# Performance work log

Hardware: AMD Instinct MI355X
Metric: run time of the kernel (lower is better)

The kernel has to match this reference:

```python
import jax, jax.numpy as jnp
import numpy as np

EPS = 1e-06
TOP_K = 2


def setup_inputs() -> dict:
    key = jax.random.key(0)
    k1, k2 = jax.random.split(key)
    B, S, H, E = 4, 4096, 2048, 64
    x = jax.random.normal(k1, (B, S, H), dtype=jnp.float32)
    per_dim_scale = jnp.ones((H,), dtype=jnp.float32)
    W = jax.random.normal(k2, (H, E), dtype=jnp.float32) * 0.02  # Dense kernel [H, E]
    return {"x": x, "per_dim_scale": per_dim_scale, "W": W}


def reference(x, per_dim_scale, W):
    H = x.shape[-1]
    x_flat = x.reshape(-1, H)  # [T, H]
    # Parameter-free RMSNorm (Gemma4VNorm)
    normed = x_flat * jax.lax.rsqrt(jnp.mean(jnp.square(x_flat), axis=-1, keepdims=True) + EPS)
    # scale by 1/sqrt(H), then learnable per-dim scale
    normed = normed * jnp.asarray(H, normed.dtype) ** -0.5
    normed = normed * per_dim_scale.astype(normed.dtype)
    router_logits = normed @ W  # [T, E]
    router_probs = jax.nn.softmax(router_logits.astype(jnp.float32), axis=-1).astype(x.dtype)
    top_k_probs, top_k_indices = jax.lax.top_k(router_probs, TOP_K)  # [T, k]
    denom = jnp.maximum(jnp.sum(top_k_probs, axis=-1, keepdims=True),
                        jnp.asarray(1e-09, top_k_probs.dtype))
    top_k_probs = top_k_probs / denom
    # Sparse dispatch weights [T, E] (sum of scaled one-hots == scatter-add)
    T = router_probs.shape[0]
    rows = jnp.arange(T)[:, None]  # [T, 1] broadcast against [T, k]
    dispatch_weights = jnp.zeros_like(router_probs).at[rows, top_k_indices].add(top_k_probs)
    return dispatch_weights
```

## Files before the change

kernel.cpp:

```cpp
#include <hip/hip_runtime.h>
#include <math.h>

#define H 2048
#define E 64
#define TAU 1e-6f

#define MT 16
#define KS 128
#define NSTEP (H / KS)
#define LPITCH 136

#define RB 16
#define CB 512
#define NCH (H / CB)
#define PITCH 516

#define WHI_OFF 65792u
#define WFRAG_BYTES 262144u
#define WLO_OFF (WHI_OFF + WFRAG_BYTES)
#define WS_NEEDED ((size_t)(WLO_OFF + WFRAG_BYTES))

typedef __attribute__((ext_vector_type(8))) short short8;
typedef __attribute__((ext_vector_type(4))) float f32x4;

__device__ __forceinline__ unsigned short bf16_rne(float f) {
    unsigned u = __float_as_uint(f);
    unsigned r = u + 0x7fffu + ((u >> 16) & 1u);
    return (unsigned short)(r >> 16);
}

__global__ __launch_bounds__(256)
void prep_w(const float* __restrict__ Wm, int* __restrict__ flags,
            unsigned short* __restrict__ whi, unsigned short* __restrict__ wlo)
{
    const int tid = blockIdx.x * 256 + threadIdx.x;
    if (tid == 0) flags[0] = 0;
    const int lane = tid & 63;
    const int fb   = tid >> 6;
    const int kc   = fb >> 2;
    const int n    = fb & 3;
    const int r0   = kc * 32 + (lane >> 4) * 8;
    const int col  = n * 16 + (lane & 15);

    short8 hv, lv;
#pragma unroll
    for (int j = 0; j < 8; ++j) {
        const float w = Wm[(r0 + j) * E + col];
        const unsigned short hb = bf16_rne(w);
        const float hf = __uint_as_float((unsigned)hb << 16);
        const unsigned short lb = bf16_rne(w - hf);
        hv[j] = (short)hb;
        lv[j] = (short)lb;
    }
    *(short8*)(whi + (size_t)tid * 8) = hv;
    *(short8*)(wlo + (size_t)tid * 8) = lv;
}

__global__ __launch_bounds__(256, 2)
void router_mfma16(const float* __restrict__ x,
                   const float* __restrict__ pds,
                   const unsigned short* __restrict__ whi,
                   const unsigned short* __restrict__ wlo,
                   float* __restrict__ out,
                   int* __restrict__ flags)
{
    __shared__ __align__(16) unsigned short yhi[MT * LPITCH];
    __shared__ __align__(16) unsigned short ylo[MT * LPITCH];
    __shared__ float lbuf[MT * E];
    __shared__ float ssbuf[256];
    __shared__ float sfac[MT];

    const int t    = threadIdx.x;
    const int wid  = t >> 6;
    const int lane = t & 63;
    const int row0 = blockIdx.x * MT;

    const int srow = t >> 4;
    const int scol = (t & 15) * 8;
    const float* xrow = x + (size_t)(row0 + srow) * H;

    f32x4 acc = {0.f, 0.f, 0.f, 0.f};
    float sumsq = 0.0f;

    float4 xv0 = *(const float4*)(xrow + scol);
    float4 xv1 = *(const float4*)(xrow + scol + 4);

    short8 whA[4], wlA[4], whB[4], wlB[4];
#pragma unroll
    for (int kk = 0; kk < 4; ++kk) {
        const size_t off = (((size_t)(kk * 4 + wid)) * 64 + lane) * 8;
        whA[kk] = *(const short8*)(whi + off);
        wlA[kk] = *(const short8*)(wlo + off);
    }

    auto body = [&](int c, short8 (&WH)[4], short8 (&WL)[4],
                           short8 (&NH)[4], short8 (&NL)[4]) {
        const int cn = (c + 1 < NSTEP) ? c + 1 : c;
#pragma unroll
        for (int kk = 0; kk < 4; ++kk) {
            const size_t off = (((size_t)((cn * 4 + kk) * 4 + wid)) * 64 + lane) * 8;
            NH[kk] = *(const short8*)(whi + off);
            NL[kk] = *(const short8*)(wlo + off);
        }

        const float* pb = pds + c * KS + scol;
        const float4 p0 = *(const float4*)(pb);
        const float4 p1 = *(const float4*)(pb + 4);
        sumsq += xv0.x * xv0.x + xv0.y * xv0.y + xv0.z * xv0.z + xv0.w * xv0.w
               + xv1.x * xv1.x + xv1.y * xv1.y + xv1.z * xv1.z + xv1.w * xv1.w;
        float y[8] = { xv0.x * p0.x, xv0.y * p0.y, xv0.z * p0.z, xv0.w * p0.w,
                       xv1.x * p1.x, xv1.y * p1.y, xv1.z * p1.z, xv1.w * p1.w };
        short8 hv, lv;
#pragma unroll
        for (int e = 0; e < 8; ++e) {
            const unsigned short hb = bf16_rne(y[e]);
            const unsigned short lb = bf16_rne(y[e] - __uint_as_float((unsigned)hb << 16));
            hv[e] = (short)hb;
            lv[e] = (short)lb;
        }
        *(short8*)(&yhi[srow * LPITCH + scol]) = hv;
        *(short8*)(&ylo[srow * LPITCH + scol]) = lv;
        __syncthreads();

        const int cx = (c + 1 < NSTEP) ? c + 1 : c;
        xv0 = *(const float4*)(xrow + cx * KS + scol);
        xv1 = *(const float4*)(xrow + cx * KS + scol + 4);

        const int abase = (lane & 15) * LPITCH + (lane >> 4) * 8;
#pragma unroll
        for (int kk = 0; kk < 4; ++kk) {
            const short8 ah = *(const short8*)(&yhi[abase + kk * 32]);
            const short8 al = *(const short8*)(&ylo[abase + kk * 32]);
            acc = __builtin_amdgcn_mfma_f32_16x16x32_bf16(ah, WH[kk], acc, 0, 0, 0);
            acc = __builtin_amdgcn_mfma_f32_16x16x32_bf16(ah, WL[kk], acc, 0, 0, 0);
            acc = __builtin_amdgcn_mfma_f32_16x16x32_bf16(al, WH[kk], acc, 0, 0, 0);
        }
        __syncthreads();
    };

    for (int c = 0; c < NSTEP; c += 2) {
        body(c,     whA, wlA, whB, wlB);
        body(c + 1, whB, wlB, whA, wlA);
    }

    ssbuf[t] = sumsq;
    __syncthreads();
    if (t < MT) {
        float tot = 0.0f;
#pragma unroll
        for (int i = 0; i < 16; ++i) tot += ssbuf[t * 16 + i];
        sfac[t] = rsqrtf(tot * (1.0f / (float)H) + 1e-6f) * 0.022097086912079608f;
    }

#pragma unroll
    for (int q = 0; q < 4; ++q)
        lbuf[(((lane >> 4) * 4) + q) * E + wid * 16 + (lane & 15)] = acc[q];
    __syncthreads();

#pragma unroll
    for (int rr = 0; rr < 4; ++rr) {
        const int r = wid * 4 + rr;
        const float L = lbuf[r * E + lane] * sfac[r];

        float m = L;
#pragma unroll
        for (int off = 32; off >= 1; off >>= 1)
            m = fmaxf(m, __shfl_xor(m, off));
        const float ev = expf(L - m);
        float S = ev;
#pragma unroll
        for (int off = 32; off >= 1; off >>= 1)
            S += __shfl_xor(S, off);
        const float p = ev / S;

        float v1 = p; int i1 = lane;
#pragma unroll
        for (int off = 32; off >= 1; off >>= 1) {
            const float ov = __shfl_xor(v1, off);
            const int   oi = __shfl_xor(i1, off);
            if (ov > v1 || (ov == v1 && oi < i1)) { v1 = ov; i1 = oi; }
        }
        float v2 = (lane == i1) ? -1.0f : p; int i2 = lane;
#pragma unroll
        for (int off = 32; off >= 1; off >>= 1) {
            const float ov = __shfl_xor(v2, off);
            const int   oi = __shfl_xor(i2, off);
            if (ov > v2 || (ov == v2 && oi < i2)) { v2 = ov; i2 = oi; }
        }
        float v3 = (lane == i1 || lane == i2) ? -1.0f : p;
#pragma unroll
        for (int off = 32; off >= 1; off >>= 1)
            v3 = fmaxf(v3, __shfl_xor(v3, off));

        if (lane == 0 && (v2 - v3) < TAU) {
            const int k = atomicAdd(flags, 1);
            flags[1 + k] = row0 + r;
        }

        const float denom = fmaxf(v1 + v2, 1e-9f);
        const float wA = v1 / denom;
        const float wB = v2 / denom;
        const float o  = (lane == i1) ? wA : ((lane == i2) ? wB : 0.0f);
        out[(size_t)(row0 + r) * E + lane] = o;
    }
}

__global__ __launch_bounds__(256)
void router_fix(const float* __restrict__ x,
                const float* __restrict__ pds,
                const float* __restrict__ Wm,
                float* __restrict__ out,
                const int* __restrict__ flags)
{
    __shared__ double yd[H];
    __shared__ double parts[4 * E];
    __shared__ double ss[256];

    const int t = threadIdx.x;
    const int count = flags[0];

    for (int j = blockIdx.x; j < count; j += gridDim.x) {
        const int r = flags[1 + j];
        const float* xr = x + (size_t)r * H;

        double s = 0.0;
#pragma unroll
        for (int i = 0; i < 8; ++i) {
            const int h = t * 8 + i;
            const double xv = (double)xr[h];
            s += xv * xv;
            yd[h] = xv * (double)pds[h];
        }
        ss[t] = s;
        __syncthreads();

        const int ex = t & 63;
        const int sl = t >> 6;
        const float* wp = Wm + (size_t)(sl * 512) * E + ex;
        double acc = 0.0;
#pragma unroll 8
        for (int h = 0; h < 512; ++h)
            acc = fma(yd[sl * 512 + h], (double)wp[(size_t)h * E], acc);
        parts[sl * E + ex] = acc;
        __syncthreads();

        if (t < 64) {
            const int lane = t;
            double tot = ss[lane * 4] + ss[lane * 4 + 1] + ss[lane * 4 + 2] + ss[lane * 4 + 3];
#pragma unroll
            for (int off = 32; off >= 1; off >>= 1)
                tot += __shfl_xor(tot, off);
            const double sf = (1.0 / sqrt(tot * (1.0 / (double)H) + 1e-6)) * 0.022097086912079608;

            const double Ld = parts[0 * E + lane] + parts[1 * E + lane]
                            + parts[2 * E + lane] + parts[3 * E + lane];
            const float L = (float)(Ld * sf);

            float m = L;
#pragma unroll
            for (int off = 32; off >= 1; off >>= 1)
                m = fmaxf(m, __shfl_xor(m, off));
            const float ev = (float)exp((double)(L - m));
            float S = ev;
#pragma unroll
            for (int off = 32; off >= 1; off >>= 1)
                S += __shfl_xor(S, off);
            const float p = ev / S;

            float v1 = p; int i1 = lane;
#pragma unroll
            for (int off = 32; off >= 1; off >>= 1) {
                const float ov = __shfl_xor(v1, off);
                const int   oi = __shfl_xor(i1, off);
                if (ov > v1 || (ov == v1 && oi < i1)) { v1 = ov; i1 = oi; }
            }
            float v2 = (lane == i1) ? -1.0f : p; int i2 = lane;
#pragma unroll
            for (int off = 32; off >= 1; off >>= 1) {
                const float ov = __shfl_xor(v2, off);
                const int   oi = __shfl_xor(i2, off);
                if (ov > v2 || (ov == v2 && oi < i2)) { v2 = ov; i2 = oi; }
            }

            const float denom = fmaxf(v1 + v2, 1e-9f);
            const float wA = v1 / denom;
            const float wB = v2 / denom;
            const float o  = (lane == i1) ? wA : ((lane == i2) ? wB : 0.0f);
            out[(size_t)r * E + lane] = o;
        }
        __syncthreads();
    }
}

__global__ void zero_cnt(int* __restrict__ flags) {
    if (threadIdx.x == 0 && blockIdx.x == 0) flags[0] = 0;
}

__global__ __launch_bounds__(256)
void router_f32(const float* __restrict__ x,
                const float* __restrict__ pds,
                const float* __restrict__ Wm,
                float* __restrict__ out,
                int* __restrict__ flags)
{
    __shared__ __align__(16) float yb[RB * PITCH];
    __shared__ float ssbuf[256];
    __shared__ float sfac[RB];

    const int t    = threadIdx.x;
    const int wv_i = t >> 6;
    const int lane = t & 63;
    const int g    = lane >> 4;
    const int e0   = (lane & 15) << 2;

    const int row0 = blockIdx.x * RB;
    const int srow = t >> 4;
    const int sseg = t & 15;

    const float* xrow = x + (size_t)(row0 + srow) * H;

    float acc[4][4];
#pragma unroll
    for (int a = 0; a < 4; ++a)
#pragma unroll
        for (int b = 0; b < 4; ++b) acc[a][b] = 0.0f;

    float sumsq = 0.0f;
    float4 xv[8];
#pragma unroll
    for (int i = 0; i < 8; ++i)
        xv[i] = *(const float4*)(xrow + sseg * 4 + i * 64);

    for (int c = 0; c < NCH; ++c) {
        const float* pbase = pds + c * CB;
#pragma unroll
        for (int i = 0; i < 8; ++i) {
            const int hl = sseg * 4 + i * 64;
            const float4 a4 = xv[i];
            const float4 p4 = *(const float4*)(pbase + hl);
            sumsq += a4.x * a4.x + a4.y * a4.y + a4.z * a4.z + a4.w * a4.w;
            float4 y4;
            y4.x = a4.x * p4.x; y4.y = a4.y * p4.y;
            y4.z = a4.z * p4.z; y4.w = a4.w * p4.w;
            *(float4*)(&yb[srow * PITCH + hl]) = y4;
        }
        __syncthreads();

        if (c + 1 < NCH) {
            const int h0n = (c + 1) * CB;
#pragma unroll
            for (int i = 0; i < 8; ++i)
                xv[i] = *(const float4*)(xrow + h0n + sseg * 4 + i * 64);
        }

        const int hb = wv_i * 128;
        const float* wbase = Wm + (size_t)(c * CB) * E + e0;
#pragma unroll 2
        for (int s = 0; s < 32; ++s) {
            const int hh = hb + s * 4;
            const float4 w0 = *(const float4*)(wbase + (size_t)(hh + 0) * E);
            const float4 w1 = *(const float4*)(wbase + (size_t)(hh + 1) * E);
            const float4 w2 = *(const float4*)(wbase + (size_t)(hh + 2) * E);
            const float4 w3 = *(const float4*)(wbase + (size_t)(hh + 3) * E);
#pragma unroll
            for (int rr = 0; rr < 4; ++rr) {
                const float4 y4 = *(const float4*)(&yb[(4 * rr + g) * PITCH + hh]);
                acc[rr][0] = fmaf(y4.w, w3.x, fmaf(y4.z, w2.x, fmaf(y4.y, w1.x, fmaf(y4.x, w0.x, acc[rr][0]))));
                acc[rr][1] = fmaf(y4.w, w3.y, fmaf(y4.z, w2.y, fmaf(y4.y, w1.y, fmaf(y4.x, w0.y, acc[rr][1]))));
                acc[rr][2] = fmaf(y4.w, w3.z, fmaf(y4.z, w2.z, fmaf(y4.y, w1.z, fmaf(y4.x, w0.z, acc[rr][2]))));
                acc[rr][3] = fmaf(y4.w, w3.w, fmaf(y4.z, w2.w, fmaf(y4.y, w1.w, fmaf(y4.x, w0.w, acc[rr][3]))));
            }
        }
        __syncthreads();
    }

    ssbuf[t] = sumsq;
    __syncthreads();
    if (t < RB) {
        float tot = 0.0f;
#pragma unroll
        for (int i = 0; i < 16; ++i) tot += ssbuf[t * 16 + i];
        sfac[t] = rsqrtf(tot * (1.0f / (float)H) + 1e-6f) * 0.022097086912079608f;
    }

#pragma unroll
    for (int rr = 0; rr < 4; ++rr) {
        const int r = 4 * rr + g;
        *(float4*)(&yb[((wv_i * RB) + r) * E + e0]) =
            make_float4(acc[rr][0], acc[rr][1], acc[rr][2], acc[rr][3]);
    }
    __syncthreads();

#pragma unroll
    for (int rr = 0; rr < 4; ++rr) {
        const int r = wv_i * 4 + rr;
        float L = yb[(0 * RB + r) * E + lane] + yb[(1 * RB + r) * E + lane]
                + yb[(2 * RB + r) * E + lane] + yb[(3 * RB + r) * E + lane];
        L *= sfac[r];

        float m = L;
#pragma unroll
        for (int off = 32; off >= 1; off >>= 1)
            m = fmaxf(m, __shfl_xor(m, off));
        const float ev = expf(L - m);
        float S = ev;
#pragma unroll
        for (int off = 32; off >= 1; off >>= 1)
            S += __shfl_xor(S, off);
        const float p = ev / S;

        float v1 = p; int i1 = lane;
#pragma unroll
        for (int off = 32; off >= 1; off >>= 1) {
            const float ov = __shfl_xor(v1, off);
            const int   oi = __shfl_xor(i1, off);
            if (ov > v1 || (ov == v1 && oi < i1)) { v1 = ov; i1 = oi; }
        }
        float v2 = (lane == i1) ? -1.0f : p; int i2 = lane;
#pragma unroll
        for (int off = 32; off >= 1; off >>= 1) {
            const float ov = __shfl_xor(v2, off);
            const int   oi = __shfl_xor(i2, off);
            if (ov > v2 || (ov == v2 && oi < i2)) { v2 = ov; i2 = oi; }
        }
        float v3 = (lane == i1 || lane == i2) ? -1.0f : p;
#pragma unroll
        for (int off = 32; off >= 1; off >>= 1)
            v3 = fmaxf(v3, __shfl_xor(v3, off));

        if (lane == 0 && (v2 - v3) < TAU) {
            const int k = atomicAdd(flags, 1);
            flags[1 + k] = row0 + r;
        }

        const float denom = fmaxf(v1 + v2, 1e-9f);
        const float wA = v1 / denom;
        const float wB = v2 / denom;
        const float o  = (lane == i1) ? wA : ((lane == i2) ? wB : 0.0f);
        out[(size_t)(row0 + r) * E + lane] = o;
    }
}

extern "C" void kernel_launch(void* const* d_in, const int* in_sizes, int n_in,
                              void* d_out, int out_size, void* d_ws, size_t ws_size,
                              hipStream_t stream) {
    const float* x   = (const float*)d_in[0];
    const float* pds = (const float*)d_in[1];
    const float* Wm  = (const float*)d_in[2];
    float* out = (float*)d_out;
    int* flags = (int*)d_ws;

    const int T = in_sizes[0] / H;

    if (ws_size >= WS_NEEDED) {
        unsigned short* whi = (unsigned short*)((char*)d_ws + WHI_OFF);
        unsigned short* wlo = (unsigned short*)((char*)d_ws + WLO_OFF);
        hipLaunchKernelGGL(prep_w,        dim3(64),     dim3(256), 0, stream, Wm, flags, whi, wlo);
        hipLaunchKernelGGL(router_mfma16, dim3(T / MT), dim3(256), 0, stream, x, pds, whi, wlo, out, flags);
        hipLaunchKernelGGL(router_fix,    dim3(128),    dim3(256), 0, stream, x, pds, Wm, out, flags);
    } else {
        hipLaunchKernelGGL(zero_cnt,      dim3(1),      dim3(64),  0, stream, flags);
        hipLaunchKernelGGL(router_f32,    dim3(T / RB), dim3(256), 0, stream, x, pds, Wm, out, flags);
        hipLaunchKernelGGL(router_fix,    dim3(128),    dim3(256), 0, stream, x, pds, Wm, out, flags);
    }
}
```

Before: 85.94 us.

## Split K across waves to remove per-step block barriers in router MFMA kernel

```diff
diff --git a/kernel.cpp b/kernel.cpp
--- a/kernel.cpp
+++ b/kernel.cpp
@@ -6,9 +6,7 @@
 #define TAU 1e-6f
 
 #define MT 16
-#define KS 128
-#define NSTEP (H / KS)
-#define LPITCH 136
+#define NST 4
 
 #define RB 16
 #define CB 512
@@ -57,110 +55,128 @@
 }
 
 __global__ __launch_bounds__(256, 2)
-void router_mfma16(const float* __restrict__ x,
-                   const float* __restrict__ pds,
-                   const unsigned short* __restrict__ whi,
-                   const unsigned short* __restrict__ wlo,
-                   float* __restrict__ out,
-                   int* __restrict__ flags)
+void router_nb(const float* __restrict__ x,
+               const float* __restrict__ pds,
+               const unsigned short* __restrict__ whi,
+               const unsigned short* __restrict__ wlo,
+               float* __restrict__ out,
+               int* __restrict__ flags)
 {
-    __shared__ __align__(16) unsigned short yhi[MT * LPITCH];
-    __shared__ __align__(16) unsigned short ylo[MT * LPITCH];
-    __shared__ float lbuf[MT * E];
-    __shared__ float ssbuf[256];
-    __shared__ float sfac[MT];
+    __shared__ __align__(16) unsigned short ybuf[4][2][4][520];
+    __shared__ float ssbuf[64];
+    __shared__ float sfac[16];
 
     const int t    = threadIdx.x;
     const int wid  = t >> 6;
     const int lane = t & 63;
+    const int lgrp = lane >> 4;
+    const int lsub = lane & 15;
     const int row0 = blockIdx.x * MT;
 
-    const int srow = t >> 4;
-    const int scol = (t & 15) * 8;
-    const float* xrow = x + (size_t)(row0 + srow) * H;
-
-    f32x4 acc = {0.f, 0.f, 0.f, 0.f};
-    float sumsq = 0.0f;
-
-    float4 xv0 = *(const float4*)(xrow + scol);
-    float4 xv1 = *(const float4*)(xrow + scol + 4);
-
-    short8 whA[4], wlA[4], whB[4], wlB[4];
-#pragma unroll
-    for (int kk = 0; kk < 4; ++kk) {
-        const size_t off = (((size_t)(kk * 4 + wid)) * 64 + lane) * 8;
-        whA[kk] = *(const short8*)(whi + off);
-        wlA[kk] = *(const short8*)(wlo + off);
-    }
-
-    auto body = [&](int c, short8 (&WH)[4], short8 (&WL)[4],
-                           short8 (&NH)[4], short8 (&NL)[4]) {
-        const int cn = (c + 1 < NSTEP) ? c + 1 : c;
-#pragma unroll
-        for (int kk = 0; kk < 4; ++kk) {
-            const size_t off = (((size_t)((cn * 4 + kk) * 4 + wid)) * 64 + lane) * 8;
-            NH[kk] = *(const short8*)(whi + off);
-            NL[kk] = *(const short8*)(wlo + off);
-        }
-
-        const float* pb = pds + c * KS + scol;
-        const float4 p0 = *(const float4*)(pb);
+    const int kcl_w  = lsub >> 2;
+    const int koff_w = (lsub & 3) * 8;
+    const int kbase  = wid * 512;
+
+    f32x4 acc[4] = {{0.f,0.f,0.f,0.f},{0.f,0.f,0.f,0.f},
+                    {0.f,0.f,0.f,0.f},{0.f,0.f,0.f,0.f}};
+    float sq[4] = {0.f, 0.f, 0.f, 0.f};
+
+    float4 xv[4][2];
+#pragma unroll
+    for (int rr = 0; rr < 4; ++rr) {
+        const float* p = x + (size_t)(row0 + rr * 4 + lgrp) * H + kbase + lsub * 8;
+        xv[rr][0] = *(const float4*)p;
+        xv[rr][1] = *(const float4*)(p + 4);
+    }
+
+    for (int st = 0; st < NST; ++st) {
+        const float* pb = pds + kbase + st * 128 + lsub * 8;
+        const float4 p0 = *(const float4*)pb;
         const float4 p1 = *(const float4*)(pb + 4);
-        sumsq += xv0.x * xv0.x + xv0.y * xv0.y + xv0.z * xv0.z + xv0.w * xv0.w
-               + xv1.x * xv1.x + xv1.y * xv1.y + xv1.z * xv1.z + xv1.w * xv1.w;
-        float y[8] = { xv0.x * p0.x, xv0.y * p0.y, xv0.z * p0.z, xv0.w * p0.w,
-                       xv1.x * p1.x, xv1.y * p1.y, xv1.z * p1.z, xv1.w * p1.w };
-        short8 hv, lv;
-#pragma unroll
-        for (int e = 0; e < 8; ++e) {
-            const unsigned short hb = bf16_rne(y[e]);
-            const unsigned short lb = bf16_rne(y[e] - __uint_as_float((unsigned)hb << 16));
-            hv[e] = (short)hb;
-            lv[e] = (short)lb;
-        }
-        *(short8*)(&yhi[srow * LPITCH + scol]) = hv;
-        *(short8*)(&ylo[srow * LPITCH + scol]) = lv;
-        __syncthreads();
-
-        const int cx = (c + 1 < NSTEP) ? c + 1 : c;
-        xv0 = *(const float4*)(xrow + cx * KS + scol);
-        xv1 = *(const float4*)(xrow + cx * KS + scol + 4);
-
-        const int abase = (lane & 15) * LPITCH + (lane >> 4) * 8;
-#pragma unroll
-        for (int kk = 0; kk < 4; ++kk) {
-            const short8 ah = *(const short8*)(&yhi[abase + kk * 32]);
-            const short8 al = *(const short8*)(&ylo[abase + kk * 32]);
-            acc = __builtin_amdgcn_mfma_f32_16x16x32_bf16(ah, WH[kk], acc, 0, 0, 0);
-            acc = __builtin_amdgcn_mfma_f32_16x16x32_bf16(ah, WL[kk], acc, 0, 0, 0);
-            acc = __builtin_amdgcn_mfma_f32_16x16x32_bf16(al, WH[kk], acc, 0, 0, 0);
-        }
-        __syncthreads();
-    };
-
-    for (int c = 0; c < NSTEP; c += 2) {
-        body(c,     whA, wlA, whB, wlB);
-        body(c + 1, whB, wlB, whA, wlA);
-    }
-
-    ssbuf[t] = sumsq;
+#pragma unroll
+        for (int rr = 0; rr < 4; ++rr) {
+            const float4 a0 = xv[rr][0];
+            const float4 a1 = xv[rr][1];
+            sq[rr] += a0.x * a0.x + a0.y * a0.y + a0.z * a0.z + a0.w * a0.w
+                    + a1.x * a1.x + a1.y * a1.y + a1.z * a1.z + a1.w * a1.w;
+            const float y[8] = { a0.x * p0.x, a0.y * p0.y, a0.z * p0.z, a0.w * p0.w,
+                                 a1.x * p1.x, a1.y * p1.y, a1.z * p1.z, a1.w * p1.w };
+            short8 hv, lv;
+#pragma unroll
+            for (int e = 0; e < 8; ++e) {
+                const unsigned short hb = bf16_rne(y[e]);
+                const unsigned short lb = bf16_rne(y[e] - __uint_as_float((unsigned)hb << 16));
+                hv[e] = (short)hb;
+                lv[e] = (short)lb;
+            }
+            const int didx = (rr * 4 + lgrp) * 32 + koff_w;
+            *(short8*)(&ybuf[wid][0][kcl_w][didx]) = hv;
+            *(short8*)(&ybuf[wid][1][kcl_w][didx]) = lv;
+        }
+
+        if (st + 1 < NST) {
+#pragma unroll
+            for (int rr = 0; rr < 4; ++rr) {
+                const float* p = x + (size_t)(row0 + rr * 4 + lgrp) * H
+                               + kbase + (st + 1) * 128 + lsub * 8;
+                xv[rr][0] = *(const float4*)p;
+                xv[rr][1] = *(const float4*)(p + 4);
+            }
+        }
+
+        const int aoff = lsub * 32 + lgrp * 8;
+#pragma unroll
+        for (int kcl = 0; kcl < 4; ++kcl) {
+            const int kc = wid * 16 + st * 4 + kcl;
+            const unsigned short* wbh = whi + (size_t)kc * 2048 + lane * 8;
+            const unsigned short* wbl = wlo + (size_t)kc * 2048 + lane * 8;
+            short8 bh[4], bl[4];
+#pragma unroll
+            for (int n = 0; n < 4; ++n) {
+                bh[n] = *(const short8*)(wbh + n * 512);
+                bl[n] = *(const short8*)(wbl + n * 512);
+            }
+            const short8 ah = *(const short8*)(&ybuf[wid][0][kcl][aoff]);
+            const short8 al = *(const short8*)(&ybuf[wid][1][kcl][aoff]);
+#pragma unroll
+            for (int n = 0; n < 4; ++n) {
+                acc[n] = __builtin_amdgcn_mfma_f32_16x16x32_bf16(ah, bh[n], acc[n], 0, 0, 0);
+                acc[n] = __builtin_amdgcn_mfma_f32_16x16x32_bf16(ah, bl[n], acc[n], 0, 0, 0);
+                acc[n] = __builtin_amdgcn_mfma_f32_16x16x32_bf16(al, bh[n], acc[n], 0, 0, 0);
+            }
+        }
+    }
+
+    float* lb = (float*)ybuf;
+    float* lw = lb + wid * 2080;
+#pragma unroll
+    for (int n = 0; n < 4; ++n)
+#pragma unroll
+        for (int q = 0; q < 4; ++q)
+            lw[(lgrp * 4 + q) * 64 + n * 16 + lsub] = acc[n][q];
+
+#pragma unroll
+    for (int rr = 0; rr < 4; ++rr) {
+        float s = sq[rr];
+        s += __shfl_xor(s, 1);
+        s += __shfl_xor(s, 2);
+        s += __shfl_xor(s, 4);
+        s += __shfl_xor(s, 8);
+        if (lsub == 0) ssbuf[wid * 16 + rr * 4 + lgrp] = s;
+    }
     __syncthreads();
-    if (t < MT) {
-        float tot = 0.0f;
-#pragma unroll
-        for (int i = 0; i < 16; ++i) tot += ssbuf[t * 16 + i];
+
+    if (t < 16) {
+        const float tot = ssbuf[t] + ssbuf[16 + t] + ssbuf[32 + t] + ssbuf[48 + t];
         sfac[t] = rsqrtf(tot * (1.0f / (float)H) + 1e-6f) * 0.022097086912079608f;
     }
-
-#pragma unroll
-    for (int q = 0; q < 4; ++q)
-        lbuf[(((lane >> 4) * 4) + q) * E + wid * 16 + (lane & 15)] = acc[q];
     __syncthreads();
 
 #pragma unroll
     for (int rr = 0; rr < 4; ++rr) {
         const int r = wid * 4 + rr;
-        const float L = lbuf[r * E + lane] * sfac[r];
+        const float L = (lb[r * 64 + lane]        + lb[2080 + r * 64 + lane]
+                       + lb[4160 + r * 64 + lane] + lb[6240 + r * 64 + lane]) * sfac[r];
 
         float m = L;
 #pragma unroll
@@ -455,12 +471,12 @@
     if (ws_size >= WS_NEEDED) {
         unsigned short* whi = (unsigned short*)((char*)d_ws + WHI_OFF);
         unsigned short* wlo = (unsigned short*)((char*)d_ws + WLO_OFF);
-        hipLaunchKernelGGL(prep_w,        dim3(64),     dim3(256), 0, stream, Wm, flags, whi, wlo);
-        hipLaunchKernelGGL(router_mfma16, dim3(T / MT), dim3(256), 0, stream, x, pds, whi, wlo, out, flags);
-        hipLaunchKernelGGL(router_fix,    dim3(128),    dim3(256), 0, stream, x, pds, Wm, out, flags);
+        hipLaunchKernelGGL(prep_w,     dim3(64),     dim3(256), 0, stream, Wm, flags, whi, wlo);
+        hipLaunchKernelGGL(router_nb,  dim3(T / MT), dim3(256), 0, stream, x, pds, whi, wlo, out, flags);
+        hipLaunchKernelGGL(router_fix, dim3(128),    dim3(256), 0, stream, x, pds, Wm, out, flags);
     } else {
-        hipLaunchKernelGGL(zero_cnt,      dim3(1),      dim3(64),  0, stream, flags);
-        hipLaunchKernelGGL(router_f32,    dim3(T / RB), dim3(256), 0, stream, x, pds, Wm, out, flags);
-        hipLaunchKernelGGL(router_fix,    dim3(128),    dim3(256), 0, stream, x, pds, Wm, out, flags);
-    }
-}
+        hipLaunchKernelGGL(zero_cnt,   dim3(1),      dim3(64),  0, stream, flags);
+        hipLaunchKernelGGL(router_f32, dim3(T / RB), dim3(256), 0, stream, x, pds, Wm, out, flags);
+        hipLaunchKernelGGL(router_fix, dim3(128),    dim3(256), 0, stream, x, pds, Wm, out, flags);
+    }
+}
```

After: 85.90 us. Within noise of the previous version (-0.0%).
